# Kernel optimization log

Measured on AMD Instinct MI355X. Metric: run time of the kernel, lower is better.

Reference implementation:

```python
import jax, jax.numpy as jnp
import numpy as np


def _scinol_new_p(p0, S2, G, eta, M, cond):
    # SCINOL effective-parameter computation (done under no_grad in torch)
    denom = jnp.sqrt(S2 + M * M)
    theta = jnp.clip(G / denom, -1.0, 1.0)
    upd = jnp.where(cond, theta / (2.0 * denom) * eta, 0.0)
    return p0 + jax.lax.stop_gradient(upd)


def _conv(x, w, b):
    y = jax.lax.conv_general_dilated(x, w, window_strides=(1, 1), padding='VALID',
                                     dimension_numbers=('NCHW', 'OIHW', 'NCHW'))
    return y + b[None, :, None, None]


def _maxpool2(x):
    return jax.lax.reduce_window(x, -jnp.inf, jax.lax.max, (1, 1, 2, 2), (1, 1, 2, 2), 'VALID')


def _scinol_conv(x, w0, wS2, wG, weta, wM, b0, bS2, bG, beta):
    # M-update: per-input-channel mean (over batch) of max-abs over H,W
    stat = jax.lax.stop_gradient(jnp.mean(jnp.max(jnp.abs(x), axis=(2, 3)), axis=0))  # (C_in,)
    M = jnp.maximum(stat, wM)  # (C_in,)
    w = _scinol_new_p(w0, wS2, wG, weta, M[None, :, None, None], wG != 0)
    b = _scinol_new_p(b0, bS2, bG, beta, jnp.float32(1.0), bG != 0)
    return _conv(x, w, b)


def _scinol_linear(x, w0, wS2, wG, weta, wM, b0, bS2, bG, beta):
    stat = jax.lax.stop_gradient(jnp.mean(jnp.abs(x), axis=0))  # (in_features,)
    M = jnp.maximum(wM, stat)  # broadcast -> (out, in)
    w = _scinol_new_p(w0, wS2, wG, weta, M, wS2 != 0)
    b = _scinol_new_p(b0, bS2, bG, beta, jnp.float32(1.0), bS2 != 0)
    return x @ w.T + b


def setup_inputs() -> dict:
    key = jax.random.key(0)
    ks = iter(jax.random.split(key, 40))
    f32 = jnp.float32
    d = {}
    d['x'] = jax.random.normal(next(ks), (2048, 1, 28, 28), dtype=f32)
    for pre, wshape, cin in [('c1', (64, 1, 5, 5), 1), ('c2', (64, 64, 5, 5), 64)]:
        d[pre + '_w0'] = jax.random.normal(next(ks), wshape, dtype=f32) * 0.1
        d[pre + '_wS2'] = jax.random.uniform(next(ks), wshape, dtype=f32)
        d[pre + '_wG'] = jax.random.normal(next(ks), wshape, dtype=f32)
        d[pre + '_weta'] = jax.random.uniform(next(ks), wshape, dtype=f32)
        d[pre + '_wM'] = jax.random.uniform(next(ks), (cin,), dtype=f32)
        d[pre + '_b0'] = jax.random.normal(next(ks), (64,), dtype=f32) * 0.1
        d[pre + '_bS2'] = jax.random.uniform(next(ks), (64,), dtype=f32)
        d[pre + '_bG'] = jax.random.normal(next(ks), (64,), dtype=f32)
        d[pre + '_beta'] = jax.random.uniform(next(ks), (64,), dtype=f32)
    d['l_w0'] = jax.random.normal(next(ks), (10, 1024), dtype=f32) * 0.03
    d['l_wS2'] = jax.random.uniform(next(ks), (10, 1024), dtype=f32)
    d['l_wG'] = jax.random.normal(next(ks), (10, 1024), dtype=f32)
    d['l_weta'] = jax.random.uniform(next(ks), (10, 1024), dtype=f32)
    d['l_wM'] = jax.random.uniform(next(ks), (10, 1024), dtype=f32)
    d['l_b0'] = jax.random.normal(next(ks), (10,), dtype=f32) * 0.03
    d['l_bS2'] = jax.random.uniform(next(ks), (10,), dtype=f32)
    d['l_bG'] = jax.random.normal(next(ks), (10,), dtype=f32)
    d['l_beta'] = jax.random.uniform(next(ks), (10,), dtype=f32)
    return d


def reference(x,
              c1_w0, c1_wS2, c1_wG, c1_weta, c1_wM, c1_b0, c1_bS2, c1_bG, c1_beta,
              c2_w0, c2_wS2, c2_wG, c2_weta, c2_wM, c2_b0, c2_bS2, c2_bG, c2_beta,
              l_w0, l_wS2, l_wG, l_weta, l_wM, l_b0, l_bS2, l_bG, l_beta):
    h = _scinol_conv(x, c1_w0, c1_wS2, c1_wG, c1_weta, c1_wM, c1_b0, c1_bS2, c1_bG, c1_beta)
    h = _maxpool2(jax.nn.relu(h))                      # (N,64,12,12)
    h = _scinol_conv(h, c2_w0, c2_wS2, c2_wG, c2_weta, c2_wM, c2_b0, c2_bS2, c2_bG, c2_beta)
    h = _maxpool2(jax.nn.relu(h))                      # (N,64,4,4)
    h = h.reshape(h.shape[0], -1)                      # (N,1024)
    return _scinol_linear(h, l_w0, l_wS2, l_wG, l_weta, l_wM, l_b0, l_bS2, l_bG, l_beta)
```

## Files before the change

### kernel.cpp

```cpp
#include <hip/hip_runtime.h>
#include <hip/hip_bf16.h>

typedef float v4f __attribute__((ext_vector_type(4)));
typedef short v8s __attribute__((ext_vector_type(8)));

#define WS_STAT2   0
#define WS_STATL   64
#define WS_B1      1088
#define WS_B2      1152
#define WS_WL      1216
#define WS_BL      11456
#define WS_IMAX    11520
#define WS_W1F_B   54272
#define WS_WP2_B   62464
#define WS_P1_B    267264
#define WS_P2_B    38016000
#define WS_C1MAX_F 9504000
#define WS_LPART_F 66816

__global__ void k_stat1(const float* __restrict__ x, float* ws) {
    int tid = threadIdx.x;
    int wv = tid >> 6, lane = tid & 63;
    int n = blockIdx.x * 4 + wv;
    const float* p = x + n * 784;
    float m = 0.f;
    for (int i = lane; i < 784; i += 64) m = fmaxf(m, fabsf(p[i]));
#pragma unroll
    for (int off = 32; off; off >>= 1) m = fmaxf(m, __shfl_xor(m, off, 64));
    if (lane == 0) ws[WS_IMAX + n] = m;
}

__global__ void k_prepw1(const float* __restrict__ w0, const float* __restrict__ S2,
                         const float* __restrict__ G, const float* __restrict__ eta,
                         const float* __restrict__ wM,
                         const float* __restrict__ b0, const float* __restrict__ bS2,
                         const float* __restrict__ bG, const float* __restrict__ beta,
                         float* ws) {
    __shared__ float red[256];
    int tid = threadIdx.x;
    float p = 0.f;
    for (int i = tid; i < 2048; i += 256) p += ws[WS_IMAX + i];
    red[tid] = p;
    __syncthreads();
    for (int s = 128; s > 0; s >>= 1) {
        if (tid < s) red[tid] += red[tid + s];
        __syncthreads();
    }
    float M = fmaxf(red[0] * (1.f / 2048.f), wM[0]);

    int i = blockIdx.x * 256 + tid;
    if (i < 4096) {
        int j = i & 7, m16 = (i >> 3) & 15, q = (i >> 7) & 3, ot = i >> 9;
        int tap = q * 8 + j, oc = m16 * 4 + ot;
        float v = 0.f;
        if (tap < 25) {
            int s = oc * 25 + tap;
            float g = G[s];
            float den = sqrtf(S2[s] + M * M);
            float inv = 1.f / den;
            float th = fminf(fmaxf(g * inv, -1.f), 1.f);
            v = w0[s] + ((g != 0.f) ? th * 0.5f * inv * eta[s] : 0.f);
        }
        ((__hip_bfloat16*)((char*)ws + WS_W1F_B))[i] = __float2bfloat16(v);
    } else if (i < 4160) {
        int c = i - 4096;
        float g = bG[c];
        float den = sqrtf(bS2[c] + 1.f);
        float inv = 1.f / den;
        float th = fminf(fmaxf(g * inv, -1.f), 1.f);
        ws[WS_B1 + c] = b0[c] + ((g != 0.f) ? th * 0.5f * inv * beta[c] : 0.f);
    }
}

__global__ void __launch_bounds__(256)
k_conv1(const float* __restrict__ x, float* ws, __hip_bfloat16* __restrict__ pool1) {
    __shared__ __align__(16) float sX[1024];
    __shared__ int sMax[64];
    int n = blockIdx.x, tid = threadIdx.x;
    int wv = tid >> 6, lane = tid & 63;
    int m16 = lane & 15, quad = lane >> 4;

    {
        const float4* src = (const float4*)(x + (size_t)n * 784);
        float4 v = {0.f, 0.f, 0.f, 0.f};
        if (tid < 196) v = src[tid];
        ((float4*)sX)[tid] = v;
    }
    if (tid < 64) sMax[tid] = 0;

    const ushort* wfrag = (const ushort*)((const char*)ws + WS_W1F_B);
    v8s bfr[4];
#pragma unroll
    for (int ot = 0; ot < 4; ++ot)
        bfr[ot] = *(const v8s*)(wfrag + ((ot * 4 + quad) * 16 + m16) * 8);
    float4 bias = *(const float4*)(ws + WS_B1 + m16 * 4);

    int dj[8];
#pragma unroll
    for (int j = 0; j < 8; ++j) {
        int tap = quad * 8 + j;
        int u = (tap * 13) >> 6;
        dj[j] = tap + 23 * u;
    }

    int W0 = wv * 36 + (m16 >> 2);
    int wy = (W0 * 171) >> 11;
    int wx = W0 - wy * 12;
    int coff = 28 * ((m16 >> 1) & 1) + (m16 & 1);

    __syncthreads();

    float vmax[4] = {0.f, 0.f, 0.f, 0.f};
    ushort* op = (ushort*)(pool1 + (size_t)n * 9216);

    float g[8];
    {
        int base = 56 * wy + 2 * wx + coff;
#pragma unroll
        for (int j = 0; j < 8; ++j) g[j] = sX[base + dj[j]];
    }
    for (int mt = 0; mt < 9; ++mt) {
        union { v8s v; ushort us[8]; } ua;
#pragma unroll
        for (int j = 0; j < 8; ++j)
            ua.us[j] = __bfloat16_as_ushort(__float2bfloat16(g[j]));

        wx += 4;
        if (wx >= 12) { wx -= 12; ++wy; }
        if (mt < 8) {
            int nb = 56 * wy + 2 * wx + coff;
#pragma unroll
            for (int j = 0; j < 8; ++j) g[j] = sX[nb + dj[j]];
        }

        v4f z = {0.f, 0.f, 0.f, 0.f};
        v4f acc[4];
#pragma unroll
        for (int ot = 0; ot < 4; ++ot)
            acc[ot] = __builtin_amdgcn_mfma_f32_16x16x32_bf16(ua.v, bfr[ot], z, 0, 0, 0);

        int Wd = (wv * 9 + mt) * 4 + quad;
        ushort4 pk;
#pragma unroll
        for (int ot = 0; ot < 4; ++ot) {
            v4f a = acc[ot];
            float m = fmaxf(fmaxf(a[0], a[1]), fmaxf(a[2], a[3]));
            float pv = fmaxf(m + bias[ot], 0.f);
            vmax[ot] = fmaxf(vmax[ot], pv);
            ((ushort*)&pk)[ot] = __bfloat16_as_ushort(__float2bfloat16(pv));
        }
        *(ushort4*)(op + Wd * 64 + m16 * 4) = pk;
    }

#pragma unroll
    for (int ot = 0; ot < 4; ++ot) {
        float m = vmax[ot];
        m = fmaxf(m, __shfl_xor(m, 16, 64));
        m = fmaxf(m, __shfl_xor(m, 32, 64));
        if (lane < 16) atomicMax(&sMax[lane * 4 + ot], __float_as_int(m));
    }
    __syncthreads();
    if (tid < 64) ws[WS_C1MAX_F + n * 64 + tid] = __int_as_float(sMax[tid]);
}

__global__ void k_stat2red(float* ws) {
    __shared__ float red[256];
    int c = blockIdx.x, t = threadIdx.x;
    float s = 0.f;
    for (int n = t; n < 2048; n += 256) s += ws[WS_C1MAX_F + n * 64 + c];
    red[t] = s;
    __syncthreads();
    for (int k = 128; k > 0; k >>= 1) {
        if (t < k) red[t] += red[t + k];
        __syncthreads();
    }
    if (t == 0) ws[WS_STAT2 + c] = red[0] * (1.f / 2048.f);
}

__global__ void k_prepw2(const float* __restrict__ w0, const float* __restrict__ S2,
                         const float* __restrict__ G, const float* __restrict__ eta,
                         const float* __restrict__ wM,
                         const float* __restrict__ b0, const float* __restrict__ bS2,
                         const float* __restrict__ bG, const float* __restrict__ beta,
                         float* ws, __hip_bfloat16* __restrict__ wp2) {
    int i = blockIdx.x * 256 + threadIdx.x;
    int j = i & 7, m16 = (i >> 3) & 15, quad = (i >> 7) & 3;
    int ot = (i >> 9) & 3, kc = (i >> 11) & 1, uv = i >> 12;
    int oc = ot * 16 + m16, ic = kc * 32 + quad * 8 + j;
    int s = oc * 1600 + ic * 25 + uv;
    float M = fmaxf(ws[WS_STAT2 + ic], wM[ic]);
    float g = G[s];
    float den = sqrtf(S2[s] + M * M);
    float inv = 1.f / den;
    float th = fminf(fmaxf(g * inv, -1.f), 1.f);
    float v = w0[s] + ((g != 0.f) ? th * 0.5f * inv * eta[s] : 0.f);
    wp2[i] = __float2bfloat16(v);
    if (blockIdx.x == 0 && threadIdx.x < 64) {
        int c = threadIdx.x;
        float gb = bG[c];
        float den2 = sqrtf(bS2[c] + 1.f);
        float inv2 = 1.f / den2;
        float th2 = fminf(fmaxf(gb * inv2, -1.f), 1.f);
        ws[WS_B2 + c] = b0[c] + ((gb != 0.f) ? th2 * 0.5f * inv2 * beta[c] : 0.f);
    }
}

__device__ __forceinline__ void prefetch_tap(const ushort* __restrict__ wp2,
                                             ushort* swbuf, int uv, int wv, int lane) {
    const char* g = (const char*)wp2 + uv * 8192 + wv * 1024 + lane * 16;
    char* l = (char*)swbuf + wv * 1024;
#pragma unroll
    for (int j = 0; j < 4; ++j)
        __builtin_amdgcn_global_load_lds(
            (const __attribute__((address_space(1))) unsigned*)(g + j * 2048),
            (__attribute__((address_space(3))) unsigned*)(l + j * 2048),
            16, 0, 0);
}

__global__ void __launch_bounds__(128)
k_conv2(const ushort* __restrict__ pool1, const ushort* __restrict__ wp2,
        const float* __restrict__ ws, float* __restrict__ pool2) {
    __shared__ __align__(16) ushort sImg[2 * 10368];
    __shared__ __align__(16) ushort sW[2][4096];
    int tid = threadIdx.x;
    int wv = tid >> 6, lane = tid & 63;
    int n0 = blockIdx.x * 2;

    {
        const uint4* src = (const uint4*)(pool1 + (size_t)n0 * 9216);
        uint4* dst = (uint4*)sImg;
#pragma unroll
        for (int i = 0; i < 18; ++i) {
            int c = tid + i * 128;
            dst[(c >> 3) * 9 + (c & 7)] = src[c];
        }
    }
    prefetch_tap(wp2, sW[0], 0, wv, lane);

    int m16 = lane & 15, quad = lane >> 4;
    int q8 = quad * 8;
    int x0 = m16 & 7;
    int yb = m16 >> 3;
    v4f acc[4][4];
#pragma unroll
    for (int i = 0; i < 4; ++i)
#pragma unroll
        for (int j = 0; j < 4; ++j) acc[i][j] = (v4f){0.f, 0.f, 0.f, 0.f};

    __syncthreads();

    const ushort* simg = sImg + wv * 10368;
    for (int uvIdx = 0; uvIdx < 25; ++uvIdx) {
        if (uvIdx < 24) prefetch_tap(wp2, sW[(uvIdx + 1) & 1], uvIdx + 1, wv, lane);
        int u = (uvIdx * 13) >> 6;
        int v = uvIdx - u * 5;
        v8s a[2][4], bf[2][4];
#pragma unroll
        for (int kc = 0; kc < 2; ++kc)
#pragma unroll
            for (int pt = 0; pt < 4; ++pt)
                a[kc][pt] = *(const v8s*)(simg +
                    ((pt * 2 + yb + u) * 12 + x0 + v) * 72 + kc * 32 + q8);
        const ushort* wb = sW[uvIdx & 1];
#pragma unroll
        for (int kc = 0; kc < 2; ++kc)
#pragma unroll
            for (int ot = 0; ot < 4; ++ot)
                bf[kc][ot] = *(const v8s*)(wb + (((kc * 4 + ot) * 4 + quad) * 16 + m16) * 8);
#pragma unroll
        for (int kc = 0; kc < 2; ++kc)
#pragma unroll
            for (int pt = 0; pt < 4; ++pt)
#pragma unroll
                for (int ot = 0; ot < 4; ++ot)
                    acc[pt][ot] = __builtin_amdgcn_mfma_f32_16x16x32_bf16(
                        a[kc][pt], bf[kc][ot], acc[pt][ot], 0, 0, 0);
        __syncthreads();
    }

    int n = n0 + wv;
    float bv[4];
#pragma unroll
    for (int ot = 0; ot < 4; ++ot) bv[ot] = ws[WS_B2 + ot * 16 + m16];
    float* outp = pool2 + (size_t)n * 1024;
#pragma unroll
    for (int pt = 0; pt < 4; ++pt)
#pragma unroll
        for (int ot = 0; ot < 4; ++ot) {
            v4f a = acc[pt][ot];
            float m01 = fmaxf(a[0], a[1]);
            float m23 = fmaxf(a[2], a[3]);
            m01 = fmaxf(m01, __shfl_xor(m01, 32, 64));
            m23 = fmaxf(m23, __shfl_xor(m23, 32, 64));
            if (lane < 32) {
                int oc = ot * 16 + m16;
                int f = oc * 16 + pt * 4 + (quad & 1) * 2;
                outp[f] = fmaxf(m01 + bv[ot], 0.f);
                outp[f + 1] = fmaxf(m23 + bv[ot], 0.f);
            }
        }
}

__global__ void k_statl(const float* __restrict__ pool2, float* ws) {
    int b = blockIdx.x, tid = threadIdx.x;
    float4 s = {0.f, 0.f, 0.f, 0.f};
    for (int im = 0; im < 32; ++im) {
        float4 v = ((const float4*)(pool2 + (size_t)(b * 32 + im) * 1024))[tid];
        s.x += v.x; s.y += v.y; s.z += v.z; s.w += v.w;
    }
    ((float4*)(ws + WS_LPART_F + b * 1024))[tid] = s;
}

__global__ void k_statlred(float* ws) {
    int f = blockIdx.x * 256 + threadIdx.x;
    float s = 0.f;
#pragma unroll
    for (int b = 0; b < 64; ++b) s += ws[WS_LPART_F + b * 1024 + f];
    ws[WS_STATL + f] = s;
}

__global__ void k_prepwl(const float* __restrict__ w0, const float* __restrict__ S2,
                         const float* __restrict__ G, const float* __restrict__ eta,
                         const float* __restrict__ wM,
                         const float* __restrict__ b0, const float* __restrict__ bS2,
                         const float* __restrict__ bG, const float* __restrict__ beta,
                         float* ws) {
    int i = blockIdx.x * 256 + threadIdx.x;
    if (i < 10240) {
        int f = i & 1023;
        float stat = ws[WS_STATL + f] * (1.f / 2048.f);
        float M = fmaxf(wM[i], stat);
        float s2 = S2[i];
        float den = sqrtf(s2 + M * M);
        float inv = 1.f / den;
        float th = fminf(fmaxf(G[i] * inv, -1.f), 1.f);
        ws[WS_WL + i] = w0[i] + ((s2 != 0.f) ? th * 0.5f * inv * eta[i] : 0.f);
    } else if (i < 10250) {
        int c = i - 10240;
        float s2 = bS2[c];
        float den = sqrtf(s2 + 1.f);
        float inv = 1.f / den;
        float th = fminf(fmaxf(bG[c] * inv, -1.f), 1.f);
        ws[WS_BL + c] = b0[c] + ((s2 != 0.f) ? th * 0.5f * inv * beta[c] : 0.f);
    }
}

__global__ void k_linear(const float* __restrict__ pool2, const float* __restrict__ ws,
                         float* __restrict__ out) {
    int tid = threadIdx.x;
    int wv = tid >> 6, lane = tid & 63;
    int n = blockIdx.x * 4 + wv;
    const float* hp = pool2 + (size_t)n * 1024;
    float h[16];
#pragma unroll
    for (int j = 0; j < 16; ++j) h[j] = hp[j * 64 + lane];
    for (int oc = 0; oc < 10; ++oc) {
        const float* wp = ws + WS_WL + oc * 1024;
        float d = 0.f;
#pragma unroll
        for (int j = 0; j < 16; ++j) d = fmaf(h[j], wp[j * 64 + lane], d);
#pragma unroll
        for (int off = 32; off; off >>= 1) d += __shfl_xor(d, off, 64);
        if (lane == 0) out[n * 10 + oc] = d + ws[WS_BL + oc];
    }
}

extern "C" void kernel_launch(void* const* d_in, const int* in_sizes, int n_in,
                              void* d_out, int out_size, void* d_ws, size_t ws_size,
                              hipStream_t stream) {
    const float* x = (const float*)d_in[0];
    float* ws = (float*)d_ws;
    __hip_bfloat16* wp2 = (__hip_bfloat16*)((char*)d_ws + WS_WP2_B);
    __hip_bfloat16* p1 = (__hip_bfloat16*)((char*)d_ws + WS_P1_B);
    float* p2 = (float*)((char*)d_ws + WS_P2_B);
    float* out = (float*)d_out;

    k_stat1<<<512, 256, 0, stream>>>(x, ws);
    k_prepw1<<<17, 256, 0, stream>>>(
        (const float*)d_in[1], (const float*)d_in[2], (const float*)d_in[3],
        (const float*)d_in[4], (const float*)d_in[5], (const float*)d_in[6],
        (const float*)d_in[7], (const float*)d_in[8], (const float*)d_in[9], ws);
    k_conv1<<<2048, 256, 0, stream>>>(x, ws, p1);
    k_stat2red<<<64, 256, 0, stream>>>(ws);
    k_prepw2<<<400, 256, 0, stream>>>(
        (const float*)d_in[10], (const float*)d_in[11], (const float*)d_in[12],
        (const float*)d_in[13], (const float*)d_in[14], (const float*)d_in[15],
        (const float*)d_in[16], (const float*)d_in[17], (const float*)d_in[18], ws, wp2);
    k_conv2<<<1024, 128, 0, stream>>>((const ushort*)p1, (const ushort*)wp2, ws, p2);
    k_statl<<<64, 256, 0, stream>>>(p2, ws);
    k_statlred<<<4, 256, 0, stream>>>(ws);
    k_prepwl<<<41, 256, 0, stream>>>(
        (const float*)d_in[19], (const float*)d_in[20], (const float*)d_in[21],
        (const float*)d_in[22], (const float*)d_in[23], (const float*)d_in[24],
        (const float*)d_in[25], (const float*)d_in[26], (const float*)d_in[27], ws);
    k_linear<<<512, 256, 0, stream>>>(p2, ws, out);
}
```

Baseline: 220.2 us.

## Load conv2 weight taps into registers directly and fold stat reduction into prepwl

In k_conv2, the weight taps are no longer staged through LDS with global_load_lds and a per-tap __syncthreads. Each lane now loads its B fragments straight from global memory into a double-buffered register array, and the tap loop is fully unrolled. This removes 25 block barriers and the LDS weight traffic, at the cost of more VGPRs (16 v8s fragments) and global/L2 loads on the critical path. Separately, the k_statlred launch is removed and its 64-way partial-sum reduction is recomputed inside k_prepwl, so each of the 10 output rows repeats it.

```diff
diff --git a/kernel.cpp b/kernel.cpp
--- a/kernel.cpp
+++ b/kernel.cpp
@@ -205,23 +205,10 @@
     }
 }
 
-__device__ __forceinline__ void prefetch_tap(const ushort* __restrict__ wp2,
-                                             ushort* swbuf, int uv, int wv, int lane) {
-    const char* g = (const char*)wp2 + uv * 8192 + wv * 1024 + lane * 16;
-    char* l = (char*)swbuf + wv * 1024;
-#pragma unroll
-    for (int j = 0; j < 4; ++j)
-        __builtin_amdgcn_global_load_lds(
-            (const __attribute__((address_space(1))) unsigned*)(g + j * 2048),
-            (__attribute__((address_space(3))) unsigned*)(l + j * 2048),
-            16, 0, 0);
-}
-
 __global__ void __launch_bounds__(128)
 k_conv2(const ushort* __restrict__ pool1, const ushort* __restrict__ wp2,
         const float* __restrict__ ws, float* __restrict__ pool2) {
     __shared__ __align__(16) ushort sImg[2 * 10368];
-    __shared__ __align__(16) ushort sW[2][4096];
     int tid = threadIdx.x;
     int wv = tid >> 6, lane = tid & 63;
     int n0 = blockIdx.x * 2;
@@ -235,7 +222,6 @@
             dst[(c >> 3) * 9 + (c & 7)] = src[c];
         }
     }
-    prefetch_tap(wp2, sW[0], 0, wv, lane);
 
     int m16 = lane & 15, quad = lane >> 4;
     int q8 = quad * 8;
@@ -247,26 +233,37 @@
 #pragma unroll
         for (int j = 0; j < 4; ++j) acc[i][j] = (v4f){0.f, 0.f, 0.f, 0.f};
 
+    const ushort* wlane = wp2 + lane * 8;
+    v8s bf[2][2][4];
+#pragma unroll
+    for (int kc = 0; kc < 2; ++kc)
+#pragma unroll
+        for (int ot = 0; ot < 4; ++ot)
+            bf[0][kc][ot] = *(const v8s*)(wlane + (kc * 4 + ot) * 512);
+
     __syncthreads();
 
     const ushort* simg = sImg + wv * 10368;
+#pragma unroll
     for (int uvIdx = 0; uvIdx < 25; ++uvIdx) {
-        if (uvIdx < 24) prefetch_tap(wp2, sW[(uvIdx + 1) & 1], uvIdx + 1, wv, lane);
+        int cur = uvIdx & 1, nxt = cur ^ 1;
+        if (uvIdx < 24) {
+            const ushort* wnext = wlane + (uvIdx + 1) * 4096;
+#pragma unroll
+            for (int kc = 0; kc < 2; ++kc)
+#pragma unroll
+                for (int ot = 0; ot < 4; ++ot)
+                    bf[nxt][kc][ot] = *(const v8s*)(wnext + (kc * 4 + ot) * 512);
+        }
         int u = (uvIdx * 13) >> 6;
         int v = uvIdx - u * 5;
-        v8s a[2][4], bf[2][4];
+        v8s a[2][4];
 #pragma unroll
         for (int kc = 0; kc < 2; ++kc)
 #pragma unroll
             for (int pt = 0; pt < 4; ++pt)
                 a[kc][pt] = *(const v8s*)(simg +
                     ((pt * 2 + yb + u) * 12 + x0 + v) * 72 + kc * 32 + q8);
-        const ushort* wb = sW[uvIdx & 1];
-#pragma unroll
-        for (int kc = 0; kc < 2; ++kc)
-#pragma unroll
-            for (int ot = 0; ot < 4; ++ot)
-                bf[kc][ot] = *(const v8s*)(wb + (((kc * 4 + ot) * 4 + quad) * 16 + m16) * 8);
 #pragma unroll
         for (int kc = 0; kc < 2; ++kc)
 #pragma unroll
@@ -274,8 +271,7 @@
 #pragma unroll
                 for (int ot = 0; ot < 4; ++ot)
                     acc[pt][ot] = __builtin_amdgcn_mfma_f32_16x16x32_bf16(
-                        a[kc][pt], bf[kc][ot], acc[pt][ot], 0, 0, 0);
-        __syncthreads();
+                        a[kc][pt], bf[cur][kc][ot], acc[pt][ot], 0, 0, 0);
     }
 
     int n = n0 + wv;
@@ -311,14 +307,6 @@
     ((float4*)(ws + WS_LPART_F + b * 1024))[tid] = s;
 }
 
-__global__ void k_statlred(float* ws) {
-    int f = blockIdx.x * 256 + threadIdx.x;
-    float s = 0.f;
-#pragma unroll
-    for (int b = 0; b < 64; ++b) s += ws[WS_LPART_F + b * 1024 + f];
-    ws[WS_STATL + f] = s;
-}
-
 __global__ void k_prepwl(const float* __restrict__ w0, const float* __restrict__ S2,
                          const float* __restrict__ G, const float* __restrict__ eta,
                          const float* __restrict__ wM,
@@ -328,7 +316,10 @@
     int i = blockIdx.x * 256 + threadIdx.x;
     if (i < 10240) {
         int f = i & 1023;
-        float stat = ws[WS_STATL + f] * (1.f / 2048.f);
+        float s = 0.f;
+#pragma unroll
+        for (int b = 0; b < 64; ++b) s += ws[WS_LPART_F + b * 1024 + f];
+        float stat = s * (1.f / 2048.f);
         float M = fmaxf(wM[i], stat);
         float s2 = S2[i];
         float den = sqrtf(s2 + M * M);
@@ -388,7 +379,6 @@
         (const float*)d_in[16], (const float*)d_in[17], (const float*)d_in[18], ws, wp2);
     k_conv2<<<1024, 128, 0, stream>>>((const ushort*)p1, (const ushort*)wp2, ws, p2);
     k_statl<<<64, 256, 0, stream>>>(p2, ws);
-    k_statlred<<<4, 256, 0, stream>>>(ws);
     k_prepwl<<<41, 256, 0, stream>>>(
         (const float*)d_in[19], (const float*)d_in[20], (const float*)d_in[21],
         (const float*)d_in[22], (const float*)d_in[23], (const float*)d_in[24],
```

Measured after the change: 208.0 us. -5.5%, faster.
